# Kernel optimization log

Hardware: AMD Instinct MI355X
Metric: run time of the kernel (lower is better)

Reference implementation:

```python
import jax, jax.numpy as jnp
import numpy as np
from jax import lax

N, CIN, H, W = 128, 1024, 14, 14
CF, TH = 128, 128          # cv_filter, te_hidden
HP, GT, FP, A = 256, 256, 256, 32


def setup_inputs() -> dict:
    key = jax.random.key(0)
    ks = jax.random.split(key, 12)
    s = 0.05
    return {
        "image": jax.random.normal(ks[0], (N, CIN, H, W), jnp.float32),
        "code": jax.random.normal(ks[1], (N, TH), jnp.float32),
        "conv_w": jax.random.normal(ks[2], (CF, CIN, 3, 3), jnp.float32) * 0.02,
        "conv_b": jnp.zeros((CF,), jnp.float32),
        "hp_w0": jax.random.normal(ks[3], (CF + 2 + TH, HP), jnp.float32) * s,
        "hp_b0": jnp.zeros((HP,), jnp.float32),
        "hp_w1": jax.random.normal(ks[4], (HP, 1), jnp.float32) * s,
        "hp_b1": jnp.zeros((1,), jnp.float32),
        "gt_w0": jax.random.normal(ks[5], ((CF + 2) * 2 + TH, GT), jnp.float32) * s,
        "gt_b0": jnp.zeros((GT,), jnp.float32),
        "gt_w1": jax.random.normal(ks[6], (GT, GT), jnp.float32) * s,
        "gt_b1": jnp.zeros((GT,), jnp.float32),
        "fp_w0": jax.random.normal(ks[7], (GT, FP), jnp.float32) * s,
        "fp_b0": jnp.zeros((FP,), jnp.float32),
        "fp_w1": jax.random.normal(ks[8], (FP, A), jnp.float32) * s,
        "fp_b1": jnp.zeros((A,), jnp.float32),
    }


def _sarn(image, code, conv_w, conv_b, hp_w0, hp_b0, hp_w1, hp_b1,
          gt_w0, gt_b0, gt_w1, gt_b1, fp_w0, fp_b0, fp_w1, fp_b1):
    # visual_resize: 3x3 conv, stride 1, pad 1 (NCHW)
    x = lax.conv_general_dilated(image, conv_w, (1, 1), "SAME",
                                 dimension_numbers=("NCHW", "OIHW", "NCHW"))
    x = x + conv_b[None, :, None, None]                       # [n, cf, h, w]
    n, c, h, w = x.shape
    o = h * w
    # sarn_encode: append x/y coordinate channels and question code
    xc = jnp.broadcast_to(jnp.linspace(-1.0, 1.0, h).reshape(1, 1, h, 1), (n, 1, h, w))
    yc = jnp.broadcast_to(jnp.linspace(-1.0, 1.0, w).reshape(1, 1, 1, w), (n, 1, h, w))
    coord = jnp.concatenate([x, xc, yc], axis=1)              # [n, cf+2, h, w]
    q = jnp.broadcast_to(code[:, :, None, None], (n, code.shape[1], h, w))
    qenc = jnp.concatenate([coord, q], axis=1)                # [n, cf+2+th, h, w]
    ce = coord.reshape(n, c + 2, o).transpose(0, 2, 1)        # [n, o, cf+2]
    qe = qenc.reshape(n, -1, o).transpose(0, 2, 1)            # [n, o, cf+2+th]
    # h_psi: per-object attention logit
    a = jax.nn.relu(jnp.einsum("nod,dh->noh", qe, hp_w0) + hp_b0)
    att = jnp.einsum("noh,hk->nok", a, hp_w1) + hp_b1         # [n, o, 1]
    # sarn_pair: softmax select a single soft object, pair with every object
    sel = jax.nn.softmax(att[..., 0], axis=1)                 # [n, o]
    selected = jnp.einsum("no,nod->nd", sel, ce)              # [n, cf+2]
    pairs = jnp.concatenate(
        [qe, jnp.broadcast_to(selected[:, None, :], ce.shape)], axis=2)  # [n, o, 2*(cf+2)+th]
    # g_theta MLP + sum over objects
    g = jax.nn.relu(jnp.einsum("nop,pg->nog", pairs, gt_w0) + gt_b0)
    g = jax.nn.relu(jnp.einsum("nog,gk->nok", g, gt_w1) + gt_b1)
    relations = g.sum(axis=1)                                 # [n, gt]
    # f_phi MLP -> answer logits
    f = jax.nn.relu(relations @ fp_w0 + fp_b0)
    return f @ fp_w1 + fp_b1                                  # [n, a_size]


def reference(image, code, conv_w, conv_b, hp_w0, hp_b0, hp_w1, hp_b1,
              gt_w0, gt_b0, gt_w1, gt_b1, fp_w0, fp_b0, fp_w1, fp_b1):
    return _sarn(image, code, conv_w, conv_b, hp_w0, hp_b0, hp_w1, hp_b1,
                 gt_w0, gt_b0, gt_w1, gt_b1, fp_w0, fp_b0, fp_w1, fp_b1)
```

## Files before the change

kernel.cpp:

```cpp
#include <hip/hip_runtime.h>
#include <stdint.h>

typedef unsigned short u16;
typedef __bf16 bf16x8 __attribute__((ext_vector_type(8)));
typedef float f32x4 __attribute__((ext_vector_type(4)));

__device__ __forceinline__ u16 f2b(float f) {
  union { float f; uint32_t u; } v; v.f = f;
  uint32_t r = v.u + 0x7fffu + ((v.u >> 16) & 1u);
  return (u16)(r >> 16);
}
__device__ __forceinline__ float b2f(u16 b) {
  union { float f; uint32_t u; } v; v.u = ((uint32_t)b) << 16;
  return v.f;
}
__device__ __forceinline__ void g2l16(const void* g, void* l) {
  __builtin_amdgcn_global_load_lds(
      (const __attribute__((address_space(1))) void*)g,
      (__attribute__((address_space(3))) void*)l, 16, 0, 0);
}

#define N_SAMP 128
#define OPAD   224
#define ROWS   (N_SAMP * OPAD)

__global__ __launch_bounds__(256) void prep_weights(
    const float* __restrict__ conv_w, const float* __restrict__ hp_w0,
    const float* __restrict__ gt_w0, const float* __restrict__ gt_w1,
    u16* __restrict__ W2, u16* __restrict__ hp_w0t,
    u16* __restrict__ gt_w0t, u16* __restrict__ gt_w1t) {
  int idx = blockIdx.x * 256 + threadIdx.x;
  const int nW2 = 9 * 128 * 1024;
  const int nHP = 256 * 288;
  const int nGT0 = 256 * 288;
  const int nGT1 = 256 * 256;
  if (idx < nW2) {
    int s = idx / 131072; int r = idx & 131071;
    int cf = r >> 10; int cin = r & 1023;
    W2[idx] = f2b(conv_w[(cf * 1024 + cin) * 9 + s]);
    return;
  }
  idx -= nW2;
  if (idx < nHP) {
    int nn = idx / 288, kk = idx % 288;
    hp_w0t[nn * 288 + kk] = (kk < 258) ? f2b(hp_w0[kk * 256 + nn]) : (u16)0;
    return;
  }
  idx -= nHP;
  if (idx < nGT0) {
    int nn = idx / 288, kk = idx % 288;
    gt_w0t[nn * 288 + kk] = (kk < 258) ? f2b(gt_w0[kk * 256 + nn]) : (u16)0;
    return;
  }
  idx -= nGT0;
  if (idx < nGT1) {
    int nn = idx >> 8, kk = idx & 255;
    gt_w1t[nn * 256 + kk] = f2b(gt_w1[kk * 256 + nn]);
  }
}

__global__ __launch_bounds__(256) void prep_img(const float* __restrict__ image,
                                                u16* __restrict__ imgT) {
  __shared__ float t[64][197];
  int n = blockIdx.x >> 4;
  int cin0 = (blockIdx.x & 15) * 64;
  const float* src = image + ((size_t)n * 1024 + cin0) * 196;
  for (int e = threadIdx.x; e < 64 * 196; e += 256) {
    int c = e / 196, sp = e % 196;
    t[c][sp] = src[c * 196 + sp];
  }
  __syncthreads();
  int w = threadIdx.x >> 6, lane = threadIdx.x & 63;
  for (int i = 0; i < 64; ++i) {
    int spg = i * 4 + w;
    int gy = spg >> 4, gx = spg & 15;
    float v = 0.f;
    if (gy >= 1 && gy <= 14 && gx >= 1 && gx <= 14) v = t[lane][(gy - 1) * 14 + (gx - 1)];
    imgT[(((size_t)(n * 256 + spg)) << 10) + cin0 + lane] = f2b(v);
  }
}

__global__ __launch_bounds__(256) void fill_qe(const float* __restrict__ code,
                                               u16* __restrict__ qeb) {
  int base = blockIdx.x * 8;
  for (int rr = 0; rr < 8; ++rr) {
    int r = base + rr;
    int n = r / 224, o = r % 224;
    int y = o / 14, x = o % 14;
    bool valid = o < 196;
    u16* row = qeb + (size_t)r * 288;
    for (int c = threadIdx.x; c < 288; c += 256) {
      u16 v;
      if (c < 128) { if (valid) continue; v = 0; }
      else if (c == 128) v = valid ? f2b(-1.f + 2.f * y / 13.f) : (u16)0;
      else if (c == 129) v = valid ? f2b(-1.f + 2.f * x / 13.f) : (u16)0;
      else if (c < 258) v = valid ? f2b(code[n * 128 + (c - 130)]) : (u16)0;
      else v = 0;
      row[c] = v;
    }
  }
}

__global__ __launch_bounds__(256) void conv_gemm(
    const u16* __restrict__ imgT, const u16* __restrict__ W2,
    float* __restrict__ convAcc) {
  __shared__ __align__(16) u16 lA[112 * 64];
  __shared__ __align__(16) u16 lB[128 * 64];
  int tid = threadIdx.x, lane = tid & 63, w = tid >> 6;
  int wg = blockIdx.x;
  int xcd = wg & 7, grp = wg >> 3;
  int n = ((grp / 6) << 3) | xcd;
  int r6 = grp % 6;
  int oh = r6 / 3, ks = r6 % 3;
  int oBase = oh * 112;
  size_t nBase = (size_t)n << 8;
  int rowIn = lane >> 3;
  int cA = ((lane & 7) ^ rowIn) << 3;

  int yxA[4];
  for (int ii = 0; ii < 4; ++ii) {
    int t = w + ii * 4;
    int o = oBase + t * 8 + rowIn;
    bool valid = o < 196;
    int y = o / 14, x = o - y * 14;
    yxA[ii] = valid ? (y * 16 + x) : 0;
  }

  f32x4 acc[7][2];
#pragma unroll
  for (int mt = 0; mt < 7; ++mt)
#pragma unroll
    for (int j = 0; j < 2; ++j) acc[mt][j] = (f32x4){0.f, 0.f, 0.f, 0.f};

  int l = lane & 15, q = lane >> 4;
  for (int si = 0; si < 3; ++si) {
    int s = ks * 3 + si;
    int off = (s / 3) * 16 + (s % 3);
    const u16* Ws = W2 + ((size_t)(s * 128) << 10);
    for (int cb = 0; cb < 16; ++cb) {
      int k0 = cb << 6;
      __syncthreads();
      g2l16(imgT + ((nBase + (size_t)(yxA[0] + off)) << 10) + k0 + cA, &lA[(w) * 512]);
      g2l16(imgT + ((nBase + (size_t)(yxA[1] + off)) << 10) + k0 + cA, &lA[(w + 4) * 512]);
      g2l16(imgT + ((nBase + (size_t)(yxA[2] + off)) << 10) + k0 + cA, &lA[(w + 8) * 512]);
      if (w < 2)
        g2l16(imgT + ((nBase + (size_t)(yxA[3] + off)) << 10) + k0 + cA, &lA[(w + 12) * 512]);
#pragma unroll
      for (int ii = 0; ii < 4; ++ii) {
        int t = w + ii * 4;
        g2l16(Ws + ((size_t)(t * 8 + rowIn) << 10) + k0 + cA, &lB[t * 512]);
      }
      __syncthreads();
#pragma unroll
      for (int kk = 0; kk < 2; ++kk) {
        int co = ((((kk << 2) | q) ^ (l & 7)) << 3);
        bf16x8 af[7];
#pragma unroll
        for (int mt = 0; mt < 7; ++mt)
          af[mt] = *(const bf16x8*)&lA[(mt * 16 + l) * 64 + co];
#pragma unroll
        for (int jj = 0; jj < 2; ++jj) {
          bf16x8 bb = *(const bf16x8*)&lB[(w * 32 + jj * 16 + l) * 64 + co];
#pragma unroll
          for (int mt = 0; mt < 7; ++mt)
            acc[mt][jj] = __builtin_amdgcn_mfma_f32_16x16x32_bf16(af[mt], bb, acc[mt][jj], 0, 0, 0);
        }
      }
    }
  }
#pragma unroll
  for (int mt = 0; mt < 7; ++mt) {
    int o = oBase + mt * 16 + q * 4;
#pragma unroll
    for (int r4 = 0; r4 < 4; ++r4) {
      if (o + r4 < 196) {
        float* dst = convAcc + (size_t)(n * 224 + o + r4) * 128 + w * 32 + l;
        atomicAdd(dst, acc[mt][0][r4]);
        atomicAdd(dst + 16, acc[mt][1][r4]);
      }
    }
  }
}

__global__ __launch_bounds__(256) void conv_fix(
    const float* __restrict__ convAcc, const float* __restrict__ conv_b,
    u16* __restrict__ qeb) {
  int idx = blockIdx.x * 256 + threadIdx.x;
  int row196 = idx >> 5;
  int c0 = (idx & 31) << 2;
  int n = row196 / 196, o = row196 - n * 196;
  size_t row = (size_t)(n * 224 + o);
  const float4 v = *(const float4*)(convAcc + (row << 7) + c0);
  const float4 b = *(const float4*)(conv_b + c0);
  ushort4 pk;
  pk.x = f2b(v.x + b.x); pk.y = f2b(v.y + b.y);
  pk.z = f2b(v.z + b.z); pk.w = f2b(v.w + b.w);
  *(ushort4*)(qeb + row * 288 + c0) = pk;
}

template <int MODE, int KP, int KC>
__global__ __launch_bounds__(256) void gemm_kernel(
    const u16* __restrict__ A, const u16* __restrict__ Bt,
    const float* __restrict__ bias, const float* __restrict__ vec,
    float* __restrict__ outF, u16* __restrict__ outB) {
  __shared__ __align__(16) u16 lA[112 * 32];
  __shared__ __align__(16) u16 lB[128 * 32];
  int tid = threadIdx.x, lane = tid & 63, w = tid >> 6;
  int bx = blockIdx.x, by = blockIdx.y;
  int r0 = bx * 112;
  int cBase = by * 128;
  int kb = (((lane & 3) ^ ((lane >> 3) & 3)) << 3);
  int rA0 = r0 + w * 16 + (lane >> 2);
  int rA1 = r0 + (w + 4) * 16 + (lane >> 2);
  bool has1 = (w < 3);
  const u16* gA0 = A + (size_t)rA0 * KP + kb;
  const u16* gA1 = A + (size_t)rA1 * KP + kb;
  int cB0 = cBase + w * 16 + (lane >> 2);
  int cB1 = cBase + (w + 4) * 16 + (lane >> 2);
  const u16* gB0 = Bt + (size_t)cB0 * KP + kb;
  const u16* gB1 = Bt + (size_t)cB1 * KP + kb;

  f32x4 acc[7][2];
#pragma unroll
  for (int mt = 0; mt < 7; ++mt)
#pragma unroll
    for (int j = 0; j < 2; ++j) acc[mt][j] = (f32x4){0.f, 0.f, 0.f, 0.f};
  int colW = w * 32;
  int l = lane & 15, q = lane >> 4;
  int co = ((q ^ ((l >> 1) & 3)) << 3);

  for (int cb = 0; cb < KC; ++cb) {
    __syncthreads();
    g2l16(gA0 + cb * 32, &lA[w * 512]);
    if (has1) g2l16(gA1 + cb * 32, &lA[(w + 4) * 512]);
    g2l16(gB0 + cb * 32, &lB[w * 512]);
    g2l16(gB1 + cb * 32, &lB[(w + 4) * 512]);
    __syncthreads();
    bf16x8 af[7];
#pragma unroll
    for (int mt = 0; mt < 7; ++mt)
      af[mt] = *(const bf16x8*)&lA[(mt * 16 + l) * 32 + co];
#pragma unroll
    for (int j = 0; j < 2; ++j) {
      bf16x8 bfr = *(const bf16x8*)&lB[(colW + j * 16 + l) * 32 + co];
#pragma unroll
      for (int mt = 0; mt < 7; ++mt)
        acc[mt][j] = __builtin_amdgcn_mfma_f32_16x16x32_bf16(af[mt], bfr, acc[mt][j], 0, 0, 0);
    }
  }

  int q4 = lane >> 4, c = lane & 15;
  if (MODE == 0) {
    float attp[7][4];
#pragma unroll
    for (int mt = 0; mt < 7; ++mt)
#pragma unroll
      for (int r = 0; r < 4; ++r) attp[mt][r] = 0.f;
#pragma unroll
    for (int j = 0; j < 2; ++j) {
      int col = cBase + colW + j * 16 + c;
      float b0 = bias[col], w1 = vec[col];
#pragma unroll
      for (int mt = 0; mt < 7; ++mt)
#pragma unroll
        for (int r = 0; r < 4; ++r) {
          float v = fmaxf(acc[mt][j][r] + b0, 0.f);
          attp[mt][r] += v * w1;
        }
    }
#pragma unroll
    for (int mt = 0; mt < 7; ++mt)
#pragma unroll
      for (int r = 0; r < 4; ++r) {
        float p = attp[mt][r];
        p += __shfl_xor(p, 1, 64);
        p += __shfl_xor(p, 2, 64);
        p += __shfl_xor(p, 4, 64);
        p += __shfl_xor(p, 8, 64);
        if (c == 0) atomicAdd(&outF[r0 + mt * 16 + q4 * 4 + r], p);
      }
  } else if (MODE == 1) {
    int n = bx >> 1;
#pragma unroll
    for (int mt = 0; mt < 7; ++mt)
#pragma unroll
      for (int j = 0; j < 2; ++j) {
        int col = cBase + colW + j * 16 + c;
        float b = bias[n * 256 + col];
#pragma unroll
        for (int r = 0; r < 4; ++r) {
          int row = r0 + mt * 16 + q4 * 4 + r;
          outB[(size_t)row * 256 + col] = f2b(fmaxf(acc[mt][j][r] + b, 0.f));
        }
      }
  } else {
    int n = bx >> 1;
    int ob = (bx & 1) * 112;
#pragma unroll
    for (int j = 0; j < 2; ++j) {
      int col = cBase + colW + j * 16 + c;
      float b = bias[col];
      float sum = 0.f;
#pragma unroll
      for (int mt = 0; mt < 7; ++mt)
#pragma unroll
        for (int r = 0; r < 4; ++r) {
          int o = ob + mt * 16 + q4 * 4 + r;
          if (o < 196) sum += fmaxf(acc[mt][j][r] + b, 0.f);
        }
      sum += __shfl_xor(sum, 16, 64);
      sum += __shfl_xor(sum, 32, 64);
      if (q4 == 0) atomicAdd(&outF[n * 256 + col], sum);
    }
  }
}

__global__ __launch_bounds__(256) void sel_kernel(
    const float* __restrict__ att, const u16* __restrict__ qeb,
    const float* __restrict__ gt_w0, const float* __restrict__ gt_b0,
    float* __restrict__ bias2) {
  int n = blockIdx.x, t = threadIdx.x;
  int w = t >> 6, lane = t & 63;
  __shared__ u16 sq[196][130];
  __shared__ float sm[196];
  __shared__ float sel[130];
  __shared__ float red[8];
  const u16* base = qeb + (size_t)n * 224 * 288;
  for (int o = w; o < 196; o += 4) {
    const u16* rowp = base + (size_t)o * 288;
    for (int c = lane; c < 130; c += 64) sq[o][c] = rowp[c];
  }
  float a = (t < 196) ? att[n * 224 + t] : -1e30f;
  float m = a;
  for (int mask = 1; mask < 64; mask <<= 1) m = fmaxf(m, __shfl_xor(m, mask, 64));
  if (lane == 0) red[w] = m;
  __syncthreads();
  float M = fmaxf(fmaxf(red[0], red[1]), fmaxf(red[2], red[3]));
  float e = (t < 196) ? expf(a - M) : 0.f;
  float sAcc = e;
  for (int mask = 1; mask < 64; mask <<= 1) sAcc += __shfl_xor(sAcc, mask, 64);
  if (lane == 0) red[4 + w] = sAcc;
  __syncthreads();
  float S = red[4] + red[5] + red[6] + red[7];
  if (t < 196) sm[t] = e / S;
  __syncthreads();
  if (t < 130) {
    float acc = 0.f;
    for (int o = 0; o < 196; ++o) acc += sm[o] * b2f(sq[o][t]);
    sel[t] = acc;
  }
  __syncthreads();
  float acc2 = gt_b0[t];
  for (int d = 0; d < 130; ++d) acc2 += sel[d] * gt_w0[(258 + d) * 256 + t];
  bias2[n * 256 + t] = acc2;
}

__global__ __launch_bounds__(256) void fphi(
    const float* __restrict__ relations, const float* __restrict__ fp_w0,
    const float* __restrict__ fp_b0, const float* __restrict__ fp_w1,
    const float* __restrict__ fp_b1, float* __restrict__ out) {
  int n = blockIdx.x, t = threadIdx.x;
  __shared__ float rel[256];
  __shared__ float f[256];
  rel[t] = relations[n * 256 + t];
  __syncthreads();
  float acc = fp_b0[t];
  for (int k = 0; k < 256; ++k) acc += rel[k] * fp_w0[k * 256 + t];
  f[t] = fmaxf(acc, 0.f);
  __syncthreads();
  if (t < 32) {
    float o = fp_b1[0];
    for (int k = 0; k < 256; ++k) o += f[k] * fp_w1[k * 32 + t];
    out[n * 32 + t] = o;
  }
}

extern "C" void kernel_launch(void* const* d_in, const int* in_sizes, int n_in,
                              void* d_out, int out_size, void* d_ws, size_t ws_size,
                              hipStream_t stream) {
  const float* image = (const float*)d_in[0];
  const float* code = (const float*)d_in[1];
  const float* conv_w = (const float*)d_in[2];
  const float* conv_b = (const float*)d_in[3];
  const float* hp_w0 = (const float*)d_in[4];
  const float* hp_b0 = (const float*)d_in[5];
  const float* hp_w1 = (const float*)d_in[6];
  const float* gt_w0 = (const float*)d_in[8];
  const float* gt_b0 = (const float*)d_in[9];
  const float* gt_w1 = (const float*)d_in[10];
  const float* gt_b1 = (const float*)d_in[11];
  const float* fp_w0 = (const float*)d_in[12];
  const float* fp_b0 = (const float*)d_in[13];
  const float* fp_w1 = (const float*)d_in[14];
  const float* fp_b1 = (const float*)d_in[15];
  float* out = (float*)d_out;

  char* p = (char*)d_ws;
  u16* imgT = (u16*)p;   p += (size_t)128 * 256 * 1024 * 2;
  u16* W2 = (u16*)p;     p += (size_t)9 * 128 * 1024 * 2;
  u16* qeb = (u16*)p;    p += (size_t)ROWS * 288 * 2;
  u16* hp_w0t = (u16*)p; p += (size_t)256 * 288 * 2;
  u16* gt_w0t = (u16*)p; p += (size_t)256 * 288 * 2;
  u16* gt_w1t = (u16*)p; p += (size_t)256 * 256 * 2;
  float* att = (float*)p;   p += (size_t)ROWS * 4;
  float* bias2 = (float*)p; p += (size_t)128 * 256 * 4;
  float* convAcc = (float*)p; p += (size_t)ROWS * 128 * 4;
  float* relations = (float*)p; p += (size_t)128 * 256 * 4;
  u16* g1 = (u16*)convAcc;

  hipMemsetAsync(att, 0, (size_t)ROWS * 4, stream);
  hipMemsetAsync(relations, 0, (size_t)128 * 256 * 4, stream);
  hipMemsetAsync(convAcc, 0, (size_t)ROWS * 128 * 4, stream);

  prep_weights<<<5440, 256, 0, stream>>>(conv_w, hp_w0, gt_w0, gt_w1, W2, hp_w0t, gt_w0t, gt_w1t);
  prep_img<<<2048, 256, 0, stream>>>(image, imgT);
  fill_qe<<<ROWS / 8, 256, 0, stream>>>(code, qeb);
  conv_gemm<<<768, 256, 0, stream>>>(imgT, W2, convAcc);
  conv_fix<<<3136, 256, 0, stream>>>(convAcc, conv_b, qeb);
  gemm_kernel<0, 288, 9><<<dim3(256, 2), 256, 0, stream>>>(qeb, hp_w0t, hp_b0, hp_w1, att, nullptr);
  sel_kernel<<<128, 256, 0, stream>>>(att, qeb, gt_w0, gt_b0, bias2);
  gemm_kernel<1, 288, 9><<<dim3(256, 2), 256, 0, stream>>>(qeb, gt_w0t, bias2, nullptr, nullptr, g1);
  gemm_kernel<2, 256, 8><<<dim3(256, 2), 256, 0, stream>>>(g1, gt_w1t, gt_b1, nullptr, relations, nullptr);
  fphi<<<128, 256, 0, stream>>>(relations, fp_w0, fp_b0, fp_w1, fp_b1, out);
}
```

Baseline: 412.9 us.

## Fuse all stages into one persistent kernel with global barriers

Replaces ten separate launches and three memsets with a single persistent 512-block kernel whose stages are separated by software grid barriers built on atomics. The conv GEMM is resplit from 768 blocks over 3 tap groups to 512 blocks over 2 channel halves. The prep, transpose and selection stages are also vectorised or parallelised. This removes launch gaps and tail effects. In exchange it depends on all 512 blocks being co-resident, relies on a spin barrier with a timeout, and leaves stages such as the 128-block sel and fphi running on a quarter of the grid.

```diff
diff --git a/kernel.cpp b/kernel.cpp
--- a/kernel.cpp
+++ b/kernel.cpp
@@ -4,6 +4,12 @@
 typedef unsigned short u16;
 typedef __bf16 bf16x8 __attribute__((ext_vector_type(8)));
 typedef float f32x4 __attribute__((ext_vector_type(4)));
+typedef unsigned short u16x8 __attribute__((ext_vector_type(8)));
+
+#define NBLK 512
+#define N_SAMP 128
+#define OPAD   224
+#define ROWS   (N_SAMP * OPAD)
 
 __device__ __forceinline__ u16 f2b(float f) {
   union { float f; uint32_t u; } v; v.f = f;
@@ -20,107 +26,116 @@
       (__attribute__((address_space(3))) void*)l, 16, 0, 0);
 }
 
-#define N_SAMP 128
-#define OPAD   224
-#define ROWS   (N_SAMP * OPAD)
-
-__global__ __launch_bounds__(256) void prep_weights(
-    const float* __restrict__ conv_w, const float* __restrict__ hp_w0,
-    const float* __restrict__ gt_w0, const float* __restrict__ gt_w1,
-    u16* __restrict__ W2, u16* __restrict__ hp_w0t,
-    u16* __restrict__ gt_w0t, u16* __restrict__ gt_w1t) {
-  int idx = blockIdx.x * 256 + threadIdx.x;
-  const int nW2 = 9 * 128 * 1024;
-  const int nHP = 256 * 288;
-  const int nGT0 = 256 * 288;
-  const int nGT1 = 256 * 256;
-  if (idx < nW2) {
-    int s = idx / 131072; int r = idx & 131071;
-    int cf = r >> 10; int cin = r & 1023;
-    W2[idx] = f2b(conv_w[(cf * 1024 + cin) * 9 + s]);
-    return;
-  }
-  idx -= nW2;
-  if (idx < nHP) {
-    int nn = idx / 288, kk = idx % 288;
-    hp_w0t[nn * 288 + kk] = (kk < 258) ? f2b(hp_w0[kk * 256 + nn]) : (u16)0;
-    return;
-  }
-  idx -= nHP;
-  if (idx < nGT0) {
-    int nn = idx / 288, kk = idx % 288;
-    gt_w0t[nn * 288 + kk] = (kk < 258) ? f2b(gt_w0[kk * 256 + nn]) : (u16)0;
-    return;
-  }
-  idx -= nGT0;
-  if (idx < nGT1) {
-    int nn = idx >> 8, kk = idx & 255;
-    gt_w1t[nn * 256 + kk] = f2b(gt_w1[kk * 256 + nn]);
-  }
-}
-
-__global__ __launch_bounds__(256) void prep_img(const float* __restrict__ image,
-                                                u16* __restrict__ imgT) {
-  __shared__ float t[64][197];
-  int n = blockIdx.x >> 4;
-  int cin0 = (blockIdx.x & 15) * 64;
-  const float* src = image + ((size_t)n * 1024 + cin0) * 196;
-  for (int e = threadIdx.x; e < 64 * 196; e += 256) {
-    int c = e / 196, sp = e % 196;
-    t[c][sp] = src[c * 196 + sp];
-  }
-  __syncthreads();
-  int w = threadIdx.x >> 6, lane = threadIdx.x & 63;
-  for (int i = 0; i < 64; ++i) {
-    int spg = i * 4 + w;
-    int gy = spg >> 4, gx = spg & 15;
-    float v = 0.f;
-    if (gy >= 1 && gy <= 14 && gx >= 1 && gx <= 14) v = t[lane][(gy - 1) * 14 + (gx - 1)];
-    imgT[(((size_t)(n * 256 + spg)) << 10) + cin0 + lane] = f2b(v);
-  }
-}
-
-__global__ __launch_bounds__(256) void fill_qe(const float* __restrict__ code,
-                                               u16* __restrict__ qeb) {
-  int base = blockIdx.x * 8;
-  for (int rr = 0; rr < 8; ++rr) {
-    int r = base + rr;
-    int n = r / 224, o = r % 224;
-    int y = o / 14, x = o % 14;
-    bool valid = o < 196;
-    u16* row = qeb + (size_t)r * 288;
-    for (int c = threadIdx.x; c < 288; c += 256) {
-      u16 v;
-      if (c < 128) { if (valid) continue; v = 0; }
-      else if (c == 128) v = valid ? f2b(-1.f + 2.f * y / 13.f) : (u16)0;
-      else if (c == 129) v = valid ? f2b(-1.f + 2.f * x / 13.f) : (u16)0;
-      else if (c < 258) v = valid ? f2b(code[n * 128 + (c - 130)]) : (u16)0;
-      else v = 0;
-      row[c] = v;
-    }
-  }
-}
-
-__global__ __launch_bounds__(256) void conv_gemm(
-    const u16* __restrict__ imgT, const u16* __restrict__ W2,
-    float* __restrict__ convAcc) {
-  __shared__ __align__(16) u16 lA[112 * 64];
-  __shared__ __align__(16) u16 lB[128 * 64];
+__global__ void init_bar(int* bar) { if (threadIdx.x < 16) bar[threadIdx.x] = 0; }
+
+__device__ __forceinline__ void gbar(int* bar, int idx) {
+  __threadfence();
+  __syncthreads();
+  if (threadIdx.x == 0) {
+    atomicAdd(&bar[idx], 1);
+    int t = 0;
+    while (__hip_atomic_load(&bar[idx], __ATOMIC_ACQUIRE, __HIP_MEMORY_SCOPE_AGENT) < NBLK) {
+      __builtin_amdgcn_s_sleep(8);
+      if (++t > 3000000) break;
+    }
+  }
+  __syncthreads();
+  __threadfence();
+}
+
+__device__ void prep_img_part(char* smem, int b, const float* __restrict__ image,
+                              u16* __restrict__ imgT) {
+  float (*t)[197] = (float(*)[197])smem;
+  int tid = threadIdx.x;
+  for (int uu = 0; uu < 4; ++uu) {
+    int unit = b * 4 + uu;
+    int n = unit >> 4, cin0 = (unit & 15) << 6;
+    const float* src = image + ((size_t)n * 1024 + cin0) * 196;
+    __syncthreads();
+    for (int e = tid; e < 64 * 196; e += 256) {
+      int c = e / 196, sp = e - c * 196;
+      t[c][sp] = src[c * 196 + sp];
+    }
+    __syncthreads();
+    int cg = tid & 7, sg = tid >> 3;
+    for (int it = 0; it < 8; ++it) {
+      int spg = it * 32 + sg;
+      int gy = spg >> 4, gx = spg & 15;
+      bool valid = (gy >= 1 && gy <= 14 && gx >= 1 && gx <= 14);
+      int spi = (gy - 1) * 14 + (gx - 1);
+      u16x8 v;
+#pragma unroll
+      for (int j = 0; j < 8; ++j) v[j] = valid ? f2b(t[cg * 8 + j][spi]) : (u16)0;
+      *(u16x8*)(imgT + (((size_t)(n * 256 + spg)) << 10) + cin0 + cg * 8) = v;
+    }
+  }
+}
+
+__device__ void prep_w2(char* smem, int cf, const float* __restrict__ conv_w,
+                        u16* __restrict__ W2) {
+  float* wb = (float*)smem;
+  int tid = threadIdx.x;
+  __syncthreads();
+  for (int e = tid; e < 9216; e += 256) wb[e] = conv_w[(size_t)cf * 9216 + e];
+  __syncthreads();
+  int cin = tid * 4;
+#pragma unroll
+  for (int s = 0; s < 9; ++s) {
+    ushort4 v;
+    v.x = f2b(wb[(cin + 0) * 9 + s]);
+    v.y = f2b(wb[(cin + 1) * 9 + s]);
+    v.z = f2b(wb[(cin + 2) * 9 + s]);
+    v.w = f2b(wb[(cin + 3) * 9 + s]);
+    *(ushort4*)(W2 + (size_t)s * 131072 + cf * 1024 + cin) = v;
+  }
+}
+
+__device__ void prep_qe(char* smem, int n, const float* __restrict__ code,
+                        u16* __restrict__ qeb) {
+  u16* tmpl = (u16*)smem;
+  int tid = threadIdx.x;
+  __syncthreads();
+  if (tid < 176) {
+    int c = 128 + tid;
+    u16 v = 0;
+    if (c >= 130 && c < 258) v = f2b(code[n * 128 + c - 130]);
+    tmpl[tid] = v;
+  }
+  __syncthreads();
+  for (int it = 0; it < 16; ++it) {
+    int ch = it * 256 + tid;
+    if (ch < 3920) {
+      int o = ch / 20, j = ch - o * 20;
+      u16x8 v = *(const u16x8*)&tmpl[j * 8];
+      if (j == 0) {
+        int y = o / 14, x = o - y * 14;
+        v[0] = f2b(-1.f + 2.f * y / 13.f);
+        v[1] = f2b(-1.f + 2.f * x / 13.f);
+      }
+      *(u16x8*)(qeb + (size_t)(n * 224 + o) * 288 + 128 + j * 8) = v;
+    }
+  }
+}
+
+__device__ void conv_core(char* smem, int b, const u16* __restrict__ imgT,
+                          const u16* __restrict__ W2, float* __restrict__ convAcc) {
+  u16* lA = (u16*)smem;
+  u16* lB = (u16*)(smem + 14336);
   int tid = threadIdx.x, lane = tid & 63, w = tid >> 6;
-  int wg = blockIdx.x;
-  int xcd = wg & 7, grp = wg >> 3;
-  int n = ((grp / 6) << 3) | xcd;
-  int r6 = grp % 6;
-  int oh = r6 / 3, ks = r6 % 3;
+  int xcd = b & 7, grp = b >> 3;
+  int n = ((grp >> 2) << 3) | xcd;
+  int r4 = grp & 3;
+  int oh = r4 >> 1, ks = r4 & 1;
   int oBase = oh * 112;
   size_t nBase = (size_t)n << 8;
   int rowIn = lane >> 3;
   int cA = ((lane & 7) ^ rowIn) << 3;
 
   int yxA[4];
+#pragma unroll
   for (int ii = 0; ii < 4; ++ii) {
-    int t = w + ii * 4;
-    int o = oBase + t * 8 + rowIn;
+    int t2 = w + ii * 4;
+    int o = oBase + t2 * 8 + rowIn;
     bool valid = o < 196;
     int y = o / 14, x = o - y * 14;
     yxA[ii] = valid ? (y * 16 + x) : 0;
@@ -133,38 +148,38 @@
     for (int j = 0; j < 2; ++j) acc[mt][j] = (f32x4){0.f, 0.f, 0.f, 0.f};
 
   int l = lane & 15, q = lane >> 4;
-  for (int si = 0; si < 3; ++si) {
-    int s = ks * 3 + si;
-    int off = (s / 3) * 16 + (s % 3);
+  int kbase = ks << 9;
+  for (int u = 0; u < 72; ++u) {
+    int s = u >> 3;
+    int k0 = kbase + ((u & 7) << 6);
+    int s3 = s / 3;
+    int off = s3 * 16 + (s - s3 * 3);
     const u16* Ws = W2 + ((size_t)(s * 128) << 10);
-    for (int cb = 0; cb < 16; ++cb) {
-      int k0 = cb << 6;
-      __syncthreads();
-      g2l16(imgT + ((nBase + (size_t)(yxA[0] + off)) << 10) + k0 + cA, &lA[(w) * 512]);
-      g2l16(imgT + ((nBase + (size_t)(yxA[1] + off)) << 10) + k0 + cA, &lA[(w + 4) * 512]);
-      g2l16(imgT + ((nBase + (size_t)(yxA[2] + off)) << 10) + k0 + cA, &lA[(w + 8) * 512]);
-      if (w < 2)
-        g2l16(imgT + ((nBase + (size_t)(yxA[3] + off)) << 10) + k0 + cA, &lA[(w + 12) * 512]);
-#pragma unroll
-      for (int ii = 0; ii < 4; ++ii) {
-        int t = w + ii * 4;
-        g2l16(Ws + ((size_t)(t * 8 + rowIn) << 10) + k0 + cA, &lB[t * 512]);
-      }
-      __syncthreads();
-#pragma unroll
-      for (int kk = 0; kk < 2; ++kk) {
-        int co = ((((kk << 2) | q) ^ (l & 7)) << 3);
-        bf16x8 af[7];
+    __syncthreads();
+    g2l16(imgT + ((nBase + (size_t)(yxA[0] + off)) << 10) + k0 + cA, &lA[(w) * 512]);
+    g2l16(imgT + ((nBase + (size_t)(yxA[1] + off)) << 10) + k0 + cA, &lA[(w + 4) * 512]);
+    g2l16(imgT + ((nBase + (size_t)(yxA[2] + off)) << 10) + k0 + cA, &lA[(w + 8) * 512]);
+    if (w < 2)
+      g2l16(imgT + ((nBase + (size_t)(yxA[3] + off)) << 10) + k0 + cA, &lA[(w + 12) * 512]);
+#pragma unroll
+    for (int ii = 0; ii < 4; ++ii) {
+      int t2 = w + ii * 4;
+      g2l16(Ws + ((size_t)(t2 * 8 + rowIn) << 10) + k0 + cA, &lB[t2 * 512]);
+    }
+    __syncthreads();
+#pragma unroll
+    for (int kk = 0; kk < 2; ++kk) {
+      int co = ((((kk << 2) | q) ^ (l & 7)) << 3);
+      bf16x8 af[7];
+#pragma unroll
+      for (int mt = 0; mt < 7; ++mt)
+        af[mt] = *(const bf16x8*)&lA[(mt * 16 + l) * 64 + co];
+#pragma unroll
+      for (int jj = 0; jj < 2; ++jj) {
+        bf16x8 bb = *(const bf16x8*)&lB[(w * 32 + jj * 16 + l) * 64 + co];
 #pragma unroll
         for (int mt = 0; mt < 7; ++mt)
-          af[mt] = *(const bf16x8*)&lA[(mt * 16 + l) * 64 + co];
-#pragma unroll
-        for (int jj = 0; jj < 2; ++jj) {
-          bf16x8 bb = *(const bf16x8*)&lB[(w * 32 + jj * 16 + l) * 64 + co];
-#pragma unroll
-          for (int mt = 0; mt < 7; ++mt)
-            acc[mt][jj] = __builtin_amdgcn_mfma_f32_16x16x32_bf16(af[mt], bb, acc[mt][jj], 0, 0, 0);
-        }
+          acc[mt][jj] = __builtin_amdgcn_mfma_f32_16x16x32_bf16(af[mt], bb, acc[mt][jj], 0, 0, 0);
       }
     }
   }
@@ -172,53 +187,33 @@
   for (int mt = 0; mt < 7; ++mt) {
     int o = oBase + mt * 16 + q * 4;
 #pragma unroll
-    for (int r4 = 0; r4 < 4; ++r4) {
-      if (o + r4 < 196) {
-        float* dst = convAcc + (size_t)(n * 224 + o + r4) * 128 + w * 32 + l;
-        atomicAdd(dst, acc[mt][0][r4]);
-        atomicAdd(dst + 16, acc[mt][1][r4]);
+    for (int r4b = 0; r4b < 4; ++r4b) {
+      if (o + r4b < 196) {
+        float* dst = convAcc + (size_t)(n * 224 + o + r4b) * 128 + w * 32 + l;
+        atomicAdd(dst, acc[mt][0][r4b]);
+        atomicAdd(dst + 16, acc[mt][1][r4b]);
       }
     }
   }
 }
 
-__global__ __launch_bounds__(256) void conv_fix(
-    const float* __restrict__ convAcc, const float* __restrict__ conv_b,
-    u16* __restrict__ qeb) {
-  int idx = blockIdx.x * 256 + threadIdx.x;
-  int row196 = idx >> 5;
-  int c0 = (idx & 31) << 2;
-  int n = row196 / 196, o = row196 - n * 196;
-  size_t row = (size_t)(n * 224 + o);
-  const float4 v = *(const float4*)(convAcc + (row << 7) + c0);
-  const float4 b = *(const float4*)(conv_b + c0);
-  ushort4 pk;
-  pk.x = f2b(v.x + b.x); pk.y = f2b(v.y + b.y);
-  pk.z = f2b(v.z + b.z); pk.w = f2b(v.w + b.w);
-  *(ushort4*)(qeb + row * 288 + c0) = pk;
-}
-
-template <int MODE, int KP, int KC>
-__global__ __launch_bounds__(256) void gemm_kernel(
-    const u16* __restrict__ A, const u16* __restrict__ Bt,
-    const float* __restrict__ bias, const float* __restrict__ vec,
-    float* __restrict__ outF, u16* __restrict__ outB) {
-  __shared__ __align__(16) u16 lA[112 * 32];
-  __shared__ __align__(16) u16 lB[128 * 32];
+template <int MODE>
+__device__ void gemm_core(char* smem, int bx, int by,
+                          const u16* __restrict__ A, const u16* __restrict__ Bt,
+                          int KP, int KC,
+                          const float* __restrict__ bias, const float* __restrict__ vec,
+                          float* __restrict__ outF, u16* __restrict__ outB) {
+  u16* lA = (u16*)smem;
+  u16* lB = (u16*)(smem + 7168);
   int tid = threadIdx.x, lane = tid & 63, w = tid >> 6;
-  int bx = blockIdx.x, by = blockIdx.y;
   int r0 = bx * 112;
   int cBase = by * 128;
   int kb = (((lane & 3) ^ ((lane >> 3) & 3)) << 3);
-  int rA0 = r0 + w * 16 + (lane >> 2);
-  int rA1 = r0 + (w + 4) * 16 + (lane >> 2);
+  const u16* gA0 = A + (size_t)(r0 + w * 16 + (lane >> 2)) * KP + kb;
+  const u16* gA1 = A + (size_t)(r0 + (w + 4) * 16 + (lane >> 2)) * KP + kb;
   bool has1 = (w < 3);
-  const u16* gA0 = A + (size_t)rA0 * KP + kb;
-  const u16* gA1 = A + (size_t)rA1 * KP + kb;
-  int cB0 = cBase + w * 16 + (lane >> 2);
-  int cB1 = cBase + (w + 4) * 16 + (lane >> 2);
-  const u16* gB0 = Bt + (size_t)cB0 * KP + kb;
-  const u16* gB1 = Bt + (size_t)cB1 * KP + kb;
+  const u16* gB0 = Bt + (size_t)(cBase + w * 16 + (lane >> 2)) * KP + kb;
+  const u16* gB1 = Bt + (size_t)(cBase + (w + 4) * 16 + (lane >> 2)) * KP + kb;
 
   f32x4 acc[7][2];
 #pragma unroll
@@ -249,7 +244,6 @@
     }
   }
 
-  int q4 = lane >> 4, c = lane & 15;
   if (MODE == 0) {
     float attp[7][4];
 #pragma unroll
@@ -258,7 +252,7 @@
       for (int r = 0; r < 4; ++r) attp[mt][r] = 0.f;
 #pragma unroll
     for (int j = 0; j < 2; ++j) {
-      int col = cBase + colW + j * 16 + c;
+      int col = cBase + colW + j * 16 + l;
       float b0 = bias[col], w1 = vec[col];
 #pragma unroll
       for (int mt = 0; mt < 7; ++mt)
@@ -277,7 +271,7 @@
         p += __shfl_xor(p, 2, 64);
         p += __shfl_xor(p, 4, 64);
         p += __shfl_xor(p, 8, 64);
-        if (c == 0) atomicAdd(&outF[r0 + mt * 16 + q4 * 4 + r], p);
+        if (l == 0) atomicAdd(&outF[r0 + mt * 16 + q * 4 + r], p);
       }
   } else if (MODE == 1) {
     int n = bx >> 1;
@@ -285,12 +279,12 @@
     for (int mt = 0; mt < 7; ++mt)
 #pragma unroll
       for (int j = 0; j < 2; ++j) {
-        int col = cBase + colW + j * 16 + c;
-        float b = bias[n * 256 + col];
+        int col = cBase + colW + j * 16 + l;
+        float bb = bias[n * 256 + col];
 #pragma unroll
         for (int r = 0; r < 4; ++r) {
-          int row = r0 + mt * 16 + q4 * 4 + r;
-          outB[(size_t)row * 256 + col] = f2b(fmaxf(acc[mt][j][r] + b, 0.f));
+          int row = r0 + mt * 16 + q * 4 + r;
+          outB[(size_t)row * 256 + col] = f2b(fmaxf(acc[mt][j][r] + bb, 0.f));
         }
       }
   } else {
@@ -298,38 +292,31 @@
     int ob = (bx & 1) * 112;
 #pragma unroll
     for (int j = 0; j < 2; ++j) {
-      int col = cBase + colW + j * 16 + c;
-      float b = bias[col];
+      int col = cBase + colW + j * 16 + l;
+      float bb = bias[col];
       float sum = 0.f;
 #pragma unroll
       for (int mt = 0; mt < 7; ++mt)
 #pragma unroll
         for (int r = 0; r < 4; ++r) {
-          int o = ob + mt * 16 + q4 * 4 + r;
-          if (o < 196) sum += fmaxf(acc[mt][j][r] + b, 0.f);
+          int o = ob + mt * 16 + q * 4 + r;
+          if (o < 196) sum += fmaxf(acc[mt][j][r] + bb, 0.f);
         }
       sum += __shfl_xor(sum, 16, 64);
       sum += __shfl_xor(sum, 32, 64);
-      if (q4 == 0) atomicAdd(&outF[n * 256 + col], sum);
-    }
-  }
-}
-
-__global__ __launch_bounds__(256) void sel_kernel(
-    const float* __restrict__ att, const u16* __restrict__ qeb,
-    const float* __restrict__ gt_w0, const float* __restrict__ gt_b0,
-    float* __restrict__ bias2) {
-  int n = blockIdx.x, t = threadIdx.x;
-  int w = t >> 6, lane = t & 63;
-  __shared__ u16 sq[196][130];
-  __shared__ float sm[196];
-  __shared__ float sel[130];
-  __shared__ float red[8];
-  const u16* base = qeb + (size_t)n * 224 * 288;
-  for (int o = w; o < 196; o += 4) {
-    const u16* rowp = base + (size_t)o * 288;
-    for (int c = lane; c < 130; c += 64) sq[o][c] = rowp[c];
-  }
+      if (q == 0) atomicAdd(&outF[n * 256 + col], sum);
+    }
+  }
+}
+
+__device__ void sel_part(char* smem, int n, const float* __restrict__ att,
+                         const u16* __restrict__ qeb, const float* __restrict__ gt_w0,
+                         const float* __restrict__ gt_b0, float* __restrict__ bias2) {
+  float* sm = (float*)smem;
+  float* red = sm + 200;
+  float* part = red + 8;
+  float* sel = part + 520;
+  int t = threadIdx.x, w = t >> 6, lane = t & 63;
   float a = (t < 196) ? att[n * 224 + t] : -1e30f;
   float m = a;
   for (int mask = 1; mask < 64; mask <<= 1) m = fmaxf(m, __shfl_xor(m, mask, 64));
@@ -344,24 +331,32 @@
   float S = red[4] + red[5] + red[6] + red[7];
   if (t < 196) sm[t] = e / S;
   __syncthreads();
-  if (t < 130) {
-    float acc = 0.f;
-    for (int o = 0; o < 196; ++o) acc += sm[o] * b2f(sq[o][t]);
-    sel[t] = acc;
-  }
+  float p1 = 0.f, p2 = 0.f, p3 = 0.f;
+  for (int o = w; o < 196; o += 4) {
+    float s = sm[o];
+    const u16* row = qeb + (size_t)(n * 224 + o) * 288;
+    p1 += s * b2f(row[lane]);
+    p2 += s * b2f(row[64 + lane]);
+    if (lane < 2) p3 += s * b2f(row[128 + lane]);
+  }
+  part[w * 130 + lane] = p1;
+  part[w * 130 + 64 + lane] = p2;
+  if (lane < 2) part[w * 130 + 128 + lane] = p3;
+  __syncthreads();
+  if (t < 130) sel[t] = part[t] + part[130 + t] + part[260 + t] + part[390 + t];
   __syncthreads();
   float acc2 = gt_b0[t];
   for (int d = 0; d < 130; ++d) acc2 += sel[d] * gt_w0[(258 + d) * 256 + t];
   bias2[n * 256 + t] = acc2;
 }
 
-__global__ __launch_bounds__(256) void fphi(
-    const float* __restrict__ relations, const float* __restrict__ fp_w0,
-    const float* __restrict__ fp_b0, const float* __restrict__ fp_w1,
-    const float* __restrict__ fp_b1, float* __restrict__ out) {
-  int n = blockIdx.x, t = threadIdx.x;
-  __shared__ float rel[256];
-  __shared__ float f[256];
+__device__ void fphi_part(char* smem, int n, const float* __restrict__ relations,
+                          const float* __restrict__ fp_w0, const float* __restrict__ fp_b0,
+                          const float* __restrict__ fp_w1, const float* __restrict__ fp_b1,
+                          float* __restrict__ out) {
+  float* rel = (float*)smem;
+  float* f = rel + 256;
+  int t = threadIdx.x;
   rel[t] = relations[n * 256 + t];
   __syncthreads();
   float acc = fp_b0[t];
@@ -373,6 +368,82 @@
     for (int k = 0; k < 256; ++k) o += f[k] * fp_w1[k * 32 + t];
     out[n * 32 + t] = o;
   }
+}
+
+__global__ __launch_bounds__(256, 2) void mega(
+    const float* image, const float* code, const float* conv_w, const float* conv_b,
+    const float* hp_w0, const float* hp_b0, const float* hp_w1,
+    const float* gt_w0, const float* gt_b0, const float* gt_w1, const float* gt_b1,
+    const float* fp_w0, const float* fp_b0, const float* fp_w1, const float* fp_b1,
+    u16* imgT, u16* W2, u16* qeb, u16* hp_w0t, u16* gt_w0t, u16* gt_w1t,
+    float* att, float* bias2, float* convAcc, float* relations, float* out, int* bar) {
+  __shared__ __align__(16) char smem[50432];
+  int b = blockIdx.x, tid = threadIdx.x;
+
+  prep_img_part(smem, b, image, imgT);
+  if (b < 128) {
+    prep_w2(smem, b, conv_w, W2);
+  } else if (b < 256) {
+    prep_qe(smem, b - 128, code, qeb);
+  } else if (b < 384) {
+    int z = b - 256;
+    f32x4 zz = {0.f, 0.f, 0.f, 0.f};
+    float* za = convAcc + (size_t)z * 28672;
+#pragma unroll 4
+    for (int i2 = 0; i2 < 28; ++i2) *(f32x4*)(za + (size_t)(i2 * 256 + tid) * 4) = zz;
+    if (tid < 56) *(f32x4*)(att + (size_t)(z * 56 + tid) * 4) = zz;
+    if (tid < 64) *(f32x4*)(relations + (size_t)(z * 64 + tid) * 4) = zz;
+  } else {
+    int z = b - 384;
+    for (int e = tid; e < 576; e += 256) {
+      int idx = z * 576 + e;
+      int nn = idx / 288, kk = idx - nn * 288;
+      hp_w0t[idx] = (kk < 258) ? f2b(hp_w0[kk * 256 + nn]) : (u16)0;
+    }
+    for (int e = tid; e < 576; e += 256) {
+      int idx = z * 576 + e;
+      int nn = idx / 288, kk = idx - nn * 288;
+      gt_w0t[idx] = (kk < 258) ? f2b(gt_w0[kk * 256 + nn]) : (u16)0;
+    }
+    for (int e = tid; e < 512; e += 256) {
+      int idx = z * 512 + e;
+      int nn = idx >> 8, kk = idx & 255;
+      gt_w1t[idx] = f2b(gt_w1[kk * 256 + nn]);
+    }
+  }
+  gbar(bar, 0);
+
+  conv_core(smem, b, imgT, W2, convAcc);
+  gbar(bar, 1);
+
+  for (int u2 = b * 256 + tid; u2 < 128 * 196 * 32; u2 += NBLK * 256) {
+    int row196 = u2 >> 5;
+    int c0 = (u2 & 31) << 2;
+    int n = row196 / 196, o = row196 - n * 196;
+    size_t row = (size_t)(n * 224 + o);
+    float4 v = *(const float4*)(convAcc + (row << 7) + c0);
+    float4 bb = *(const float4*)(conv_b + c0);
+    ushort4 pk;
+    pk.x = f2b(v.x + bb.x); pk.y = f2b(v.y + bb.y);
+    pk.z = f2b(v.z + bb.z); pk.w = f2b(v.w + bb.w);
+    *(ushort4*)(qeb + row * 288 + c0) = pk;
+  }
+  gbar(bar, 2);
+
+  gemm_core<0>(smem, b & 255, b >> 8, qeb, hp_w0t, 288, 9, hp_b0, hp_w1, att, nullptr);
+  gbar(bar, 3);
+
+  if (b < 128) sel_part(smem, b, att, qeb, gt_w0, gt_b0, bias2);
+  gbar(bar, 4);
+
+  gemm_core<1>(smem, b & 255, b >> 8, qeb, gt_w0t, 288, 9, bias2, nullptr, nullptr, (u16*)convAcc);
+  gbar(bar, 5);
+
+  gemm_core<2>(smem, b & 255, b >> 8, (const u16*)convAcc, gt_w1t, 256, 8, gt_b1, nullptr,
+               relations, nullptr);
+  gbar(bar, 6);
+
+  if (b < 128) fphi_part(smem, b, relations, fp_w0, fp_b0, fp_w1, fp_b1, out);
 }
 
 extern "C" void kernel_launch(void* const* d_in, const int* in_sizes, int n_in,
@@ -406,20 +477,11 @@
   float* bias2 = (float*)p; p += (size_t)128 * 256 * 4;
   float* convAcc = (float*)p; p += (size_t)ROWS * 128 * 4;
   float* relations = (float*)p; p += (size_t)128 * 256 * 4;
-  u16* g1 = (u16*)convAcc;
-
-  hipMemsetAsync(att, 0, (size_t)ROWS * 4, stream);
-  hipMemsetAsync(relations, 0, (size_t)128 * 256 * 4, stream);
-  hipMemsetAsync(convAcc, 0, (size_t)ROWS * 128 * 4, stream);
-
-  prep_weights<<<5440, 256, 0, stream>>>(conv_w, hp_w0, gt_w0, gt_w1, W2, hp_w0t, gt_w0t, gt_w1t);
-  prep_img<<<2048, 256, 0, stream>>>(image, imgT);
-  fill_qe<<<ROWS / 8, 256, 0, stream>>>(code, qeb);
-  conv_gemm<<<768, 256, 0, stream>>>(imgT, W2, convAcc);
-  conv_fix<<<3136, 256, 0, stream>>>(convAcc, conv_b, qeb);
-  gemm_kernel<0, 288, 9><<<dim3(256, 2), 256, 0, stream>>>(qeb, hp_w0t, hp_b0, hp_w1, att, nullptr);
-  sel_kernel<<<128, 256, 0, stream>>>(att, qeb, gt_w0, gt_b0, bias2);
-  gemm_kernel<1, 288, 9><<<dim3(256, 2), 256, 0, stream>>>(qeb, gt_w0t, bias2, nullptr, nullptr, g1);
-  gemm_kernel<2, 256, 8><<<dim3(256, 2), 256, 0, stream>>>(g1, gt_w1t, gt_b1, nullptr, relations, nullptr);
-  fphi<<<128, 256, 0, stream>>>(relations, fp_w0, fp_b0, fp_w1, fp_b1, out);
-}
+  int* bar = (int*)p;    p += 64;
+
+  init_bar<<<1, 64, 0, stream>>>(bar);
+  mega<<<NBLK, 256, 0, stream>>>(image, code, conv_w, conv_b, hp_w0, hp_b0, hp_w1,
+                                 gt_w0, gt_b0, gt_w1, gt_b1, fp_w0, fp_b0, fp_w1, fp_b1,
+                                 imgT, W2, qeb, hp_w0t, gt_w0t, gt_w1t,
+                                 att, bias2, convAcc, relations, out, bar);
+}
```

After: 1.197 ms. 190% more time.
